# Performance work log

Measured on AMD Instinct MI355X. Metric: run time of the kernel, lower is better.

Reference implementation:

```python
import jax, jax.numpy as jnp
import numpy as np

B, S, F = 128, 256, 40
H, D, NH, L, FF = 64, 128, 4, 2, 2048
REG, BIN, NW = 8, 1, 3
NEG = -1e9


def _ln(x, s, b, eps=1e-5):
    m = x.mean(-1, keepdims=True)
    v = ((x - m) ** 2).mean(-1, keepdims=True)
    return (x - m) / jnp.sqrt(v + eps) * s + b


def setup_inputs() -> dict:
    key = jax.random.key(0)
    ks = list(jax.random.split(key, 40))
    k = iter(ks)
    def rn(shape, s=0.05):
        return jax.random.normal(next(k), shape, jnp.float32) * s
    inp = {}
    inp['x'] = jax.random.normal(next(k), (B, S, F), jnp.float32)
    inp['mask'] = jnp.ones((B, S, F), jnp.float32)
    inp['delta'] = jax.random.uniform(next(k), (B, S, F), jnp.float32)
    # GRU params (torch layout: [3H, in], gates order r,z,n)
    inp['gru_w_ih'] = rn((3 * H, 3 * F))
    inp['gru_w_hh'] = rn((3 * H, H))
    inp['gru_b_ih'] = rn((3 * H,))
    inp['gru_b_hh'] = rn((3 * H,))
    inp['dm_w'] = rn((D, H)); inp['dm_b'] = rn((D,))
    # transformer layers stacked on leading dim L
    inp['in_proj_w'] = rn((L, 3 * D, D)); inp['in_proj_b'] = rn((L, 3 * D))
    inp['out_proj_w'] = rn((L, D, D)); inp['out_proj_b'] = rn((L, D))
    inp['lin1_w'] = rn((L, FF, D)); inp['lin1_b'] = rn((L, FF))
    inp['lin2_w'] = rn((L, D, FF)); inp['lin2_b'] = rn((L, D))
    inp['ln1_s'] = jnp.ones((L, D), jnp.float32); inp['ln1_b'] = jnp.zeros((L, D), jnp.float32)
    inp['ln2_s'] = jnp.ones((L, D), jnp.float32); inp['ln2_b'] = jnp.zeros((L, D), jnp.float32)
    inp['score_w'] = rn((1, D)); inp['score_b'] = rn((1,))
    inp['reg_w'] = rn((NW, REG, D)); inp['reg_b'] = rn((NW, REG))
    inp['bin_w'] = rn((NW, BIN, D)); inp['bin_b'] = rn((NW, BIN))
    inp['window_id'] = jax.random.randint(next(k), (B,), 0, NW, jnp.int32)
    return inp


def reference(x, mask, delta, gru_w_ih, gru_w_hh, gru_b_ih, gru_b_hh, dm_w, dm_b,
              in_proj_w, in_proj_b, out_proj_w, out_proj_b, lin1_w, lin1_b,
              lin2_w, lin2_b, ln1_s, ln1_b, ln2_s, ln2_b, score_w, score_b,
              reg_w, reg_b, bin_w, bin_b, window_id):
    inp = jnp.concatenate([x, mask, delta], -1)          # [B,S,3F]
    xw = inp @ gru_w_ih.T + gru_b_ih                      # [B,S,3H] precomputed input gates

    def step(h, xw_t):
        gh = h @ gru_w_hh.T + gru_b_hh
        xr, xz, xn = jnp.split(xw_t, 3, -1)
        hr, hz, hn = jnp.split(gh, 3, -1)
        r = jax.nn.sigmoid(xr + hr)
        zg = jax.nn.sigmoid(xz + hz)
        n = jnp.tanh(xn + r * hn)
        h_new = (1.0 - zg) * n + zg * h
        return h_new, h_new

    h0 = jnp.zeros((x.shape[0], H), x.dtype)
    _, hs = jax.lax.scan(step, h0, jnp.swapaxes(xw, 0, 1))  # [S,B,H]
    z = jnp.swapaxes(hs, 0, 1) @ dm_w.T + dm_b              # [B,S,D]

    time_mask = mask.sum(-1) > 0                            # [B,S] bool
    bias = jnp.where(time_mask[:, None, None, :], 0.0, NEG).astype(z.dtype)
    dh = D // NH
    scale = 1.0 / np.sqrt(dh)

    for l in range(L):  # post-LN torch TransformerEncoderLayer
        qkv = z @ in_proj_w[l].T + in_proj_b[l]
        q, k, v = jnp.split(qkv, 3, -1)
        q = q.reshape(B, S, NH, dh).transpose(0, 2, 1, 3)
        k = k.reshape(B, S, NH, dh).transpose(0, 2, 1, 3)
        v = v.reshape(B, S, NH, dh).transpose(0, 2, 1, 3)
        attn = jax.nn.softmax(jnp.einsum('bhqd,bhkd->bhqk', q, k) * scale + bias, -1)
        o = jnp.einsum('bhqk,bhkd->bhqd', attn, v).transpose(0, 2, 1, 3).reshape(B, S, D)
        z = _ln(z + (o @ out_proj_w[l].T + out_proj_b[l]), ln1_s[l], ln1_b[l])
        ff = jax.nn.relu(z @ lin1_w[l].T + lin1_b[l]) @ lin2_w[l].T + lin2_b[l]
        z = _ln(z + ff, ln2_s[l], ln2_b[l])

    scores = (z @ score_w.T + score_b)[..., 0]              # [B,S]
    scores = jnp.where(time_mask, scores, NEG)
    alpha = jax.nn.softmax(scores, 1)
    pooled = jnp.einsum('bsd,bs->bd', z, alpha)             # [B,D]

    # routed heads: gather 1-of-3 head weights per sample, batched matvec
    y_reg = jnp.einsum('bod,bd->bo', reg_w[window_id], pooled) + reg_b[window_id]
    y_bin = jnp.einsum('bod,bd->bo', bin_w[window_id], pooled) + bin_b[window_id]
    return (y_reg, y_bin)
```

## Files before the change

kernel.cpp:

```cpp
#include <hip/hip_runtime.h>

typedef __attribute__((ext_vector_type(8))) short short8;
typedef __attribute__((ext_vector_type(4))) float f32x4;
typedef unsigned short u16;

#define BB   128
#define SS   256
#define FIN  40
#define HH   64
#define DD   128
#define NHH  4
#define LL   2
#define NEGV (-1e9f)

__device__ __forceinline__ u16 f2b(float f) {
    unsigned u = __float_as_uint(f);
    return (u16)((u + 0x7FFFu + ((u >> 16) & 1u)) >> 16);
}
__device__ __forceinline__ float b2f(u16 u) {
    return __uint_as_float(((unsigned)u) << 16);
}

__device__ __forceinline__ void gl_lds16(const void* g, void* s) {
    __builtin_amdgcn_global_load_lds(
        (const __attribute__((address_space(1))) void*)g,
        (__attribute__((address_space(3))) void*)s, 16, 0, 0);
}

__global__ __launch_bounds__(192) void xw_kernel(const float* __restrict__ x,
                                                 const float* __restrict__ mask,
                                                 const float* __restrict__ delta,
                                                 const float* __restrict__ w_ih,
                                                 const float* __restrict__ b_ih,
                                                 float* __restrict__ xwt) {
    __shared__ float inp[16][120];
    __shared__ float wl[192][21];
    int group = blockIdx.x >> 8;
    int t = blockIdx.x & 255;
    int tid = threadIdx.x;

    for (int idx = tid; idx < 16 * 120; idx += 192) {
        int r = idx / 120, k = idx % 120;
        size_t g = (size_t)(group * 16 + r) * 256 + t;
        float v;
        if (k < 40)      v = x[g * FIN + k];
        else if (k < 80) v = mask[g * FIN + (k - 40)];
        else             v = delta[g * FIN + (k - 80)];
        inp[r][k] = v;
    }

    float acc[16];
#pragma unroll
    for (int r = 0; r < 16; ++r) acc[r] = 0.f;

    for (int kt = 0; kt < 6; ++kt) {
        __syncthreads();
        for (int idx = tid; idx < 192 * 20; idx += 192) {
            int r = idx / 20, k = idx % 20;
            wl[r][k] = w_ih[(size_t)r * 120 + kt * 20 + k];
        }
        __syncthreads();
#pragma unroll
        for (int kk = 0; kk < 20; ++kk) {
            float w = wl[tid][kk];
            int kg = kt * 20 + kk;
#pragma unroll
            for (int r = 0; r < 16; ++r) acc[r] += w * inp[r][kg];
        }
    }
    float bias = b_ih[tid];
    float* o = xwt + ((size_t)(group * 256 + t) * 192 + tid) * 16;
#pragma unroll
    for (int r = 0; r < 16; r += 4) {
        float4 v = {acc[r] + bias, acc[r + 1] + bias, acc[r + 2] + bias, acc[r + 3] + bias};
        *(float4*)&o[r] = v;
    }
}

__device__ __forceinline__ float gru_gate(float xr, float xz, float xn,
                                          float ar, float az, float an, float hold) {
    float r  = 1.f / (1.f + __expf(-(xr + ar)));
    float zg = 1.f / (1.f + __expf(-(xz + az)));
    float nx = xn + r * an;
    float n  = 2.f / (1.f + __expf(-2.f * nx)) - 1.f;
    return (1.f - zg) * n + zg * hold;
}

__global__ __launch_bounds__(512, 1) void pre_kernel(const float* __restrict__ w_hh,
                                                     const float* __restrict__ b_hh,
                                                     const float* __restrict__ xwt,
                                                     u16* __restrict__ hsb,
                                                     const float* __restrict__ dm_w,
                                                     const float* __restrict__ ip_w,
                                                     const float* __restrict__ op_w,
                                                     const float* __restrict__ l1_w,
                                                     const float* __restrict__ l2_w,
                                                     u16* __restrict__ o_dm, u16* __restrict__ o_ip,
                                                     u16* __restrict__ o_op, u16* __restrict__ o_l1,
                                                     u16* __restrict__ o_l2,
                                                     const float* __restrict__ mask,
                                                     float* __restrict__ tm) {
    __shared__ __align__(16) u16 hb[2][16 * 64];
    __shared__ __align__(16) u16 hstage[8][16 * 64];
    int blk = blockIdx.x;
    int tid = threadIdx.x;

    if (blk >= 8) {
        if (blk < 298) {
            int cb = blk - 8;
            const float* s; u16* d; int off;
            if      (cb < 2)   { s = dm_w; d = o_dm; off = cb; }
            else if (cb < 26)  { s = ip_w; d = o_ip; off = cb - 2; }
            else if (cb < 34)  { s = op_w; d = o_op; off = cb - 26; }
            else if (cb < 162) { s = l1_w; d = o_l1; off = cb - 34; }
            else               { s = l2_w; d = o_l2; off = cb - 162; }
            int i = (off * 512 + tid) * 8;
            float4 a = *(const float4*)&s[i];
            float4 b = *(const float4*)&s[i + 4];
            short8 o;
            o[0] = (short)f2b(a.x); o[1] = (short)f2b(a.y); o[2] = (short)f2b(a.z); o[3] = (short)f2b(a.w);
            o[4] = (short)f2b(b.x); o[5] = (short)f2b(b.y); o[6] = (short)f2b(b.z); o[7] = (short)f2b(b.w);
            *(short8*)&d[i] = o;
        } else {
            int row = (blk - 298) * 512 + tid;
            if (row < BB * SS) {
                const float* m = mask + (size_t)row * FIN;
                float s = 0.f;
                for (int f = 0; f < FIN; ++f) s += m[f];
                tm[row] = (s > 0.f) ? 1.f : 0.f;
            }
        }
        return;
    }

    int b0 = blk * 16;
    int w = tid >> 6, lane = tid & 63;
    int fr = lane & 15, hi = lane >> 4;
    int cw = w & 3;
    int jg = w >> 2;

    for (int idx = tid; idx < 1024; idx += 512) hb[0][idx] = 0;

    int c = cw * 16 + fr;
    float br_ = b_hh[c], bz_ = b_hh[64 + c], bn_ = b_hh[128 + c];

    short8 wfr[2], wfz[2], wfn[2];
#pragma unroll
    for (int ks = 0; ks < 2; ++ks) {
        int slot = ks * 4 + hi;
        const float* p0 = w_hh + (size_t)c * 64 + slot * 8;
        const float* p1 = w_hh + (size_t)(64 + c) * 64 + slot * 8;
        const float* p2 = w_hh + (size_t)(128 + c) * 64 + slot * 8;
#pragma unroll
        for (int q = 0; q < 8; ++q) {
            wfr[ks][q] = (short)f2b(p0[q]);
            wfz[ks][q] = (short)f2b(p1[q]);
            wfn[ks][q] = (short)f2b(p2[q]);
        }
    }

    const float* xg = xwt + (size_t)blk * (256 * 192 * 16);
    int lo = hi * 4 + jg * 2;

    float hrA = 0.f, hrB = 0.f;

    int woA = (lo + 0) * 64 + ((((c >> 3) ^ ((lo + 0) & 7))) << 3) + (c & 7);
    int woB = (lo + 1) * 64 + ((((c >> 3) ^ ((lo + 1) & 7))) << 3) + (c & 7);
    int soA = (lo + 0) * 64 + c;
    int soB = (lo + 1) * 64 + c;

    float2 pxr[4], pxz[4], pxn[4];
#pragma unroll
    for (int u = 0; u < 4; ++u) {
        pxr[u] = *(const float2*)&xg[((size_t)u * 192 + c) * 16 + lo];
        pxz[u] = *(const float2*)&xg[((size_t)u * 192 + 64 + c) * 16 + lo];
        pxn[u] = *(const float2*)&xg[((size_t)u * 192 + 128 + c) * 16 + lo];
    }
    __syncthreads();

    int cur = 0;
    auto step = [&](float2 xr2, float2 xz2, float2 xn2, int ts) {
        f32x4 ar = {br_, br_, br_, br_};
        f32x4 az = {bz_, bz_, bz_, bz_};
        f32x4 an = {bn_, bn_, bn_, bn_};
#pragma unroll
        for (int ks = 0; ks < 2; ++ks) {
            int soff = (((ks << 2) + hi) ^ (fr & 7)) << 3;
            short8 af = *(const short8*)&hb[cur][fr * 64 + soff];
            ar = __builtin_amdgcn_mfma_f32_16x16x32_bf16(af, wfr[ks], ar, 0, 0, 0);
            az = __builtin_amdgcn_mfma_f32_16x16x32_bf16(af, wfz[ks], az, 0, 0, 0);
            an = __builtin_amdgcn_mfma_f32_16x16x32_bf16(af, wfn[ks], an, 0, 0, 0);
        }
        float aR0, aR1, aZ0, aZ1, aN0, aN1;
        if (jg == 0) { aR0 = ar[0]; aR1 = ar[1]; aZ0 = az[0]; aZ1 = az[1]; aN0 = an[0]; aN1 = an[1]; }
        else         { aR0 = ar[2]; aR1 = ar[3]; aZ0 = az[2]; aZ1 = az[3]; aN0 = an[2]; aN1 = an[3]; }
        hrA = gru_gate(xr2.x, xz2.x, xn2.x, aR0, aZ0, aN0, hrA);
        hrB = gru_gate(xr2.y, xz2.y, xn2.y, aR1, aZ1, aN1, hrB);
        u16 v0 = f2b(hrA), v1 = f2b(hrB);
        int nxt = cur ^ 1;
        hb[nxt][woA] = v0; hb[nxt][woB] = v1;
        hstage[ts][soA] = v0; hstage[ts][soB] = v1;
        asm volatile("s_waitcnt lgkmcnt(0)\n\ts_barrier" ::: "memory");
        cur = nxt;
    };

    for (int t = 0; t < SS; t += 8) {
#pragma unroll
        for (int u = 0; u < 8; ++u) {
            int tp = t + u + 4; tp = (tp < SS) ? tp : (SS - 1);
            float2 nr = *(const float2*)&xg[((size_t)tp * 192 + c) * 16 + lo];
            float2 nz = *(const float2*)&xg[((size_t)tp * 192 + 64 + c) * 16 + lo];
            float2 nn = *(const float2*)&xg[((size_t)tp * 192 + 128 + c) * 16 + lo];
            step(pxr[u & 3], pxz[u & 3], pxn[u & 3], u);
            pxr[u & 3] = nr; pxz[u & 3] = nz; pxn[u & 3] = nn;
        }
#pragma unroll
        for (int f = 0; f < 2; ++f) {
            int idx = tid + f * 512;
            int c8 = idx & 7, pair = idx >> 3;
            int ts = pair >> 4, row = pair & 15;
            short8 v = *(const short8*)&hstage[ts][row * 64 + c8 * 8];
            *(short8*)&hsb[((size_t)(b0 + row) * SS + t + ts) * 64 + c8 * 8] = v;
        }
        asm volatile("s_waitcnt lgkmcnt(0)\n\ts_barrier" ::: "memory");
    }
}

template <int MODE, bool RELU>
__global__ __launch_bounds__(256, 2) void mfma_gemm(const u16* __restrict__ A,
                                                    const u16* __restrict__ W,
                                                    const float* __restrict__ bias,
                                                    float* __restrict__ C,
                                                    u16* __restrict__ Cb,
                                                    int M, int N, int K) {
    __shared__ __align__(16) u16 Al[128 * 64];
    __shared__ __align__(16) u16 Bl[128 * 64];
    int bm = blockIdx.x, bn = blockIdx.y;
    int tid = threadIdx.x;
    int w = tid >> 6, lane = tid & 63;
    int wrow = (w >> 1) * 64, wcol = (w & 1) * 64;
    int fr = lane & 15, hi = lane >> 4;
    int rl = lane >> 3;
    int sl = lane & 7;
    int ssl = sl ^ rl;

    const u16* Ag = A + ((size_t)bm * 128) * K + ssl * 8;
    const u16* Wg = W + ((size_t)bn * 128) * K + ssl * 8;

    f32x4 acc[4][4];
#pragma unroll
    for (int i = 0; i < 4; ++i)
#pragma unroll
        for (int jj = 0; jj < 4; ++jj) acc[i][jj] = (f32x4){0.f, 0.f, 0.f, 0.f};

    int ar[4], br[4];
#pragma unroll
    for (int m = 0; m < 4; ++m) {
        ar[m] = (wrow + m * 16 + fr) * 64;
        br[m] = (wcol + m * 16 + fr) * 64;
    }
    int swz = (fr & 7);

    for (int kt = 0; kt < K; kt += 64) {
        __syncthreads();
#pragma unroll
        for (int i = 0; i < 4; ++i) {
            int c = w * 4 + i;
            int row = c * 8 + rl;
            gl_lds16(Ag + (size_t)row * K + kt, &Al[c * 512]);
            gl_lds16(Wg + (size_t)row * K + kt, &Bl[c * 512]);
        }
        __syncthreads();
#pragma unroll
        for (int kk = 0; kk < 2; ++kk) {
            short8 a[4], bq[4];
            int soff = (((kk << 2) + hi) ^ swz) << 3;
#pragma unroll
            for (int m = 0; m < 4; ++m)
                a[m] = *(const short8*)&Al[ar[m] + soff];
#pragma unroll
            for (int n = 0; n < 4; ++n)
                bq[n] = *(const short8*)&Bl[br[n] + soff];
#pragma unroll
            for (int m = 0; m < 4; ++m)
#pragma unroll
                for (int n = 0; n < 4; ++n)
                    acc[m][n] = __builtin_amdgcn_mfma_f32_16x16x32_bf16(a[m], bq[n], acc[m][n], 0, 0, 0);
        }
    }

    float bv[4];
#pragma unroll
    for (int n = 0; n < 4; ++n) bv[n] = bias[bn * 128 + wcol + n * 16 + fr];

#pragma unroll
    for (int m = 0; m < 4; ++m) {
#pragma unroll
        for (int j = 0; j < 4; ++j) {
            int row = bm * 128 + wrow + m * 16 + hi * 4 + j;
#pragma unroll
            for (int n = 0; n < 4; ++n) {
                int col = bn * 128 + wcol + n * 16 + fr;
                float vv = acc[m][n][j] + bv[n];
                if (RELU) vv = fmaxf(vv, 0.f);
                if (MODE & 1) C[(size_t)row * N + col] = vv;
                if (MODE & 2) Cb[(size_t)row * N + col] = f2b(vv);
            }
        }
    }
}

__global__ __launch_bounds__(256, 1) void tail_kernel(const u16* __restrict__ attnob,
                                                      const u16* __restrict__ opw,
                                                      const float* __restrict__ opb,
                                                      const float* __restrict__ ln1s,
                                                      const float* __restrict__ ln1b,
                                                      const u16* __restrict__ w1,
                                                      const float* __restrict__ b1,
                                                      const u16* __restrict__ w2,
                                                      const float* __restrict__ b2,
                                                      const float* __restrict__ lns,
                                                      const float* __restrict__ lnb,
                                                      float* __restrict__ z,
                                                      u16* __restrict__ zbout) {
    __shared__ __align__(16) u16 ZB[2][128 * 64];
    __shared__ __align__(16) u16 W1C[2][128 * 64];
    __shared__ __align__(16) u16 W2C[2][128 * 64];
    __shared__ __align__(16) u16 A1[2][128 * 64];
    __shared__ float lred[2][2][128];
    int bm = blockIdx.x;
    int tid = threadIdx.x;
    int w = tid >> 6, lane = tid & 63;
    int wrow = (w >> 1) * 64, wcol = (w & 1) * 64;
    int fr = lane & 15, hi = lane >> 4;
    int rl = lane >> 3, ssl = (lane & 7) ^ rl;
    int swz = fr & 7;
    int xh = wrow >> 6;

#pragma unroll
    for (int hk = 0; hk < 2; ++hk)
#pragma unroll
        for (int i = 0; i < 4; ++i) {
            int ch = w * 4 + i, row = ch * 8 + rl;
            gl_lds16(attnob + ((size_t)(bm * 128 + row)) * 128 + hk * 64 + ssl * 8, &ZB[hk][ch * 512]);
            gl_lds16(opw + ((size_t)row) * 128 + hk * 64 + ssl * 8, &W1C[hk][ch * 512]);
        }
    __syncthreads();

    {
        f32x4 acc1[4][4];
#pragma unroll
        for (int m = 0; m < 4; ++m)
#pragma unroll
            for (int n = 0; n < 4; ++n) acc1[m][n] = (f32x4){0.f, 0.f, 0.f, 0.f};
#pragma unroll
        for (int ks = 0; ks < 4; ++ks) {
            int hk = ks >> 1;
            int soff = ((((ks & 1) << 2) + hi) ^ swz) << 3;
            short8 a[4], b[4];
#pragma unroll
            for (int m = 0; m < 4; ++m)
                a[m] = *(const short8*)&ZB[hk][(wrow + m * 16 + fr) * 64 + soff];
#pragma unroll
            for (int n = 0; n < 4; ++n)
                b[n] = *(const short8*)&W1C[hk][(wcol + n * 16 + fr) * 64 + soff];
#pragma unroll
            for (int m = 0; m < 4; ++m)
#pragma unroll
                for (int n = 0; n < 4; ++n)
                    acc1[m][n] = __builtin_amdgcn_mfma_f32_16x16x32_bf16(a[m], b[n], acc1[m][n], 0, 0, 0);
        }

        float bv[4];
#pragma unroll
        for (int n = 0; n < 4; ++n) bv[n] = opb[wcol + n * 16 + fr];
        float v[4][4][4];
#pragma unroll
        for (int m = 0; m < 4; ++m)
#pragma unroll
            for (int j = 0; j < 4; ++j) {
                int row = bm * 128 + wrow + m * 16 + hi * 4 + j;
#pragma unroll
                for (int n = 0; n < 4; ++n)
                    v[m][n][j] = acc1[m][n][j] + bv[n] + z[(size_t)row * 128 + wcol + n * 16 + fr];
            }
#pragma unroll
        for (int m = 0; m < 4; ++m)
#pragma unroll
            for (int j = 0; j < 4; ++j) {
                float s = v[m][0][j] + v[m][1][j] + v[m][2][j] + v[m][3][j];
                float q = v[m][0][j]*v[m][0][j] + v[m][1][j]*v[m][1][j]
                        + v[m][2][j]*v[m][2][j] + v[m][3][j]*v[m][3][j];
#pragma unroll
                for (int off = 1; off <= 8; off <<= 1) {
                    s += __shfl_xor(s, off);
                    q += __shfl_xor(q, off);
                }
                if (fr == 0) {
                    int lrow = wrow + m * 16 + hi * 4 + j;
                    lred[0][w & 1][lrow] = s;
                    lred[1][w & 1][lrow] = q;
                }
            }
        __syncthreads();
        float sv[4], bb[4];
#pragma unroll
        for (int n = 0; n < 4; ++n) {
            sv[n] = ln1s[wcol + n * 16 + fr];
            bb[n] = ln1b[wcol + n * 16 + fr];
        }
#pragma unroll
        for (int m = 0; m < 4; ++m)
#pragma unroll
            for (int j = 0; j < 4; ++j) {
                int lrow = wrow + m * 16 + hi * 4 + j;
                float mean = (lred[0][0][lrow] + lred[0][1][lrow]) * (1.f / 128.f);
                float msq  = (lred[1][0][lrow] + lred[1][1][lrow]) * (1.f / 128.f);
                float rstd = rsqrtf(msq - mean * mean + 1e-5f);
                int row = bm * 128 + lrow;
#pragma unroll
                for (int n = 0; n < 4; ++n) {
                    int col = wcol + n * 16 + fr;
                    float o = (v[m][n][j] - mean) * rstd * sv[n] + bb[n];
                    z[(size_t)row * 128 + col] = o;
                    int e = col & 63;
                    ZB[col >> 6][lrow * 64 + ((((e >> 3) ^ (lrow & 7))) << 3) + (e & 7)] = f2b(o);
                }
            }
    }
    __syncthreads();

    f32x4 acc2[4][4];
#pragma unroll
    for (int m = 0; m < 4; ++m)
#pragma unroll
        for (int n = 0; n < 4; ++n) acc2[m][n] = (f32x4){0.f, 0.f, 0.f, 0.f};

    for (int ci = 0; ci < 16; ++ci) {
#pragma unroll
        for (int hk = 0; hk < 2; ++hk)
#pragma unroll
            for (int i = 0; i < 4; ++i) {
                int ch = w * 4 + i, row = ch * 8 + rl;
                gl_lds16(w1 + ((size_t)(ci * 128 + row)) * 128 + hk * 64 + ssl * 8, &W1C[hk][ch * 512]);
                gl_lds16(w2 + ((size_t)row) * 2048 + ci * 128 + hk * 64 + ssl * 8, &W2C[hk][ch * 512]);
            }
        __syncthreads();

        f32x4 acc1[4][4];
#pragma unroll
        for (int m = 0; m < 4; ++m)
#pragma unroll
            for (int n = 0; n < 4; ++n) acc1[m][n] = (f32x4){0.f, 0.f, 0.f, 0.f};
#pragma unroll
        for (int ks = 0; ks < 4; ++ks) {
            int hk = ks >> 1;
            int soff = ((((ks & 1) << 2) + hi) ^ swz) << 3;
            short8 a[4], b[4];
#pragma unroll
            for (int m = 0; m < 4; ++m)
                a[m] = *(const short8*)&W1C[hk][(wrow + m * 16 + fr) * 64 + soff];
#pragma unroll
            for (int n = 0; n < 4; ++n)
                b[n] = *(const short8*)&ZB[hk][(wcol + n * 16 + fr) * 64 + soff];
#pragma unroll
            for (int m = 0; m < 4; ++m)
#pragma unroll
                for (int n = 0; n < 4; ++n)
                    acc1[m][n] = __builtin_amdgcn_mfma_f32_16x16x32_bf16(a[m], b[n], acc1[m][n], 0, 0, 0);
        }
#pragma unroll
        for (int m = 0; m < 4; ++m) {
            int x0 = wrow + m * 16 + hi * 4;
            float4 bb = *(const float4*)&b1[ci * 128 + x0];
            int slot = (x0 & 63) >> 3;
            int wadd = x0 & 7;
#pragma unroll
            for (int n = 0; n < 4; ++n) {
                int r = wcol + n * 16 + fr;
                float v0 = fmaxf(acc1[m][n][0] + bb.x, 0.f);
                float v1 = fmaxf(acc1[m][n][1] + bb.y, 0.f);
                float v2 = fmaxf(acc1[m][n][2] + bb.z, 0.f);
                float v3 = fmaxf(acc1[m][n][3] + bb.w, 0.f);
                uint2 pk;
                pk.x = (unsigned)f2b(v0) | ((unsigned)f2b(v1) << 16);
                pk.y = (unsigned)f2b(v2) | ((unsigned)f2b(v3) << 16);
                *(uint2*)&A1[xh][r * 64 + ((slot ^ (r & 7)) << 3) + wadd] = pk;
            }
        }
        __syncthreads();

#pragma unroll
        for (int ks = 0; ks < 4; ++ks) {
            int hk = ks >> 1;
            int soff = ((((ks & 1) << 2) + hi) ^ swz) << 3;
            short8 a[4], b[4];
#pragma unroll
            for (int m = 0; m < 4; ++m)
                a[m] = *(const short8*)&W2C[hk][(wrow + m * 16 + fr) * 64 + soff];
#pragma unroll
            for (int n = 0; n < 4; ++n)
                b[n] = *(const short8*)&A1[hk][(wcol + n * 16 + fr) * 64 + soff];
#pragma unroll
            for (int m = 0; m < 4; ++m)
#pragma unroll
                for (int n = 0; n < 4; ++n)
                    acc2[m][n] = __builtin_amdgcn_mfma_f32_16x16x32_bf16(a[m], b[n], acc2[m][n], 0, 0, 0);
        }
        __syncthreads();
    }

    float vv[4][4][4];
#pragma unroll
    for (int m = 0; m < 4; ++m) {
        int x0 = wrow + m * 16 + hi * 4;
        float4 bb = *(const float4*)&b2[x0];
#pragma unroll
        for (int n = 0; n < 4; ++n) {
            int y = wcol + n * 16 + fr;
            float4 zo = *(const float4*)&z[((size_t)(bm * 128 + y)) * 128 + x0];
            vv[m][n][0] = acc2[m][n][0] + bb.x + zo.x;
            vv[m][n][1] = acc2[m][n][1] + bb.y + zo.y;
            vv[m][n][2] = acc2[m][n][2] + bb.z + zo.z;
            vv[m][n][3] = acc2[m][n][3] + bb.w + zo.w;
        }
    }
#pragma unroll
    for (int n = 0; n < 4; ++n) {
        float s = 0.f, q = 0.f;
#pragma unroll
        for (int m = 0; m < 4; ++m)
#pragma unroll
            for (int j = 0; j < 4; ++j) { float v = vv[m][n][j]; s += v; q += v * v; }
        s += __shfl_xor(s, 16); s += __shfl_xor(s, 32);
        q += __shfl_xor(q, 16); q += __shfl_xor(q, 32);
        if (hi == 0) {
            int y = wcol + n * 16 + fr;
            lred[0][xh][y] = s;
            lred[1][xh][y] = q;
        }
    }
    __syncthreads();
#pragma unroll
    for (int n = 0; n < 4; ++n) {
        int y = wcol + n * 16 + fr;
        float mean = (lred[0][0][y] + lred[0][1][y]) * (1.f / 128.f);
        float msq  = (lred[1][0][y] + lred[1][1][y]) * (1.f / 128.f);
        float rstd = rsqrtf(msq - mean * mean + 1e-5f);
#pragma unroll
        for (int m = 0; m < 4; ++m) {
            int x0 = wrow + m * 16 + hi * 4;
            float4 sv = *(const float4*)&lns[x0];
            float4 bv = *(const float4*)&lnb[x0];
            float o0 = (vv[m][n][0] - mean) * rstd * sv.x + bv.x;
            float o1 = (vv[m][n][1] - mean) * rstd * sv.y + bv.y;
            float o2 = (vv[m][n][2] - mean) * rstd * sv.z + bv.z;
            float o3 = (vv[m][n][3] - mean) * rstd * sv.w + bv.w;
            size_t zoff = ((size_t)(bm * 128 + y)) * 128 + x0;
            *(float4*)&z[zoff] = (float4){o0, o1, o2, o3};
            uint2 pk;
            pk.x = (unsigned)f2b(o0) | ((unsigned)f2b(o1) << 16);
            pk.y = (unsigned)f2b(o2) | ((unsigned)f2b(o3) << 16);
            *(uint2*)&zbout[zoff] = pk;
        }
    }
}

__global__ __launch_bounds__(256) void attn_mfma_kernel(const u16* __restrict__ qkv,
                                                        const float* __restrict__ tm,
                                                        u16* __restrict__ attno) {
    __shared__ __align__(16) u16 Kl[256 * 40];
    __shared__ __align__(16) u16 Vt[32 * 264];
    __shared__ __align__(16) u16 Pl[4][64 * 72];
    __shared__ float tmb[256];
    int bh = blockIdx.x;
    int b = bh >> 2, hd = bh & 3;
    int tid = threadIdx.x;
    int w = tid >> 6, lane = tid & 63;
    int fr = lane & 15, hi = lane >> 4;
    const u16* base = qkv + (size_t)b * SS * 384 + hd * 32;

    for (int idx = tid; idx < 1024; idx += 256) {
        int r = idx >> 2, s = idx & 3;
        short8 v = *(const short8*)(base + (size_t)r * 384 + 128 + s * 8);
        *(short8*)&Kl[r * 40 + s * 8] = v;
    }
    for (int idx = tid; idx < 1024; idx += 256) {
        int r = idx >> 2, s = idx & 3;
        short8 v = *(const short8*)(base + (size_t)r * 384 + 256 + s * 8);
#pragma unroll
        for (int q = 0; q < 8; ++q) Vt[(s * 8 + q) * 264 + r] = (u16)v[q];
    }
    tmb[tid] = (tm[b * SS + tid] > 0.f) ? 0.f : NEGV;

    int q0 = w * 64;
    short8 qf[4];
#pragma unroll
    for (int m = 0; m < 4; ++m)
        qf[m] = *(const short8*)(base + (size_t)(q0 + m * 16 + fr) * 384 + hi * 8);
    __syncthreads();

    const float scale = 0.17677669529663687f;
    f32x4 accO[4][2];
#pragma unroll
    for (int m = 0; m < 4; ++m) {
        accO[m][0] = (f32x4){0.f, 0.f, 0.f, 0.f};
        accO[m][1] = (f32x4){0.f, 0.f, 0.f, 0.f};
    }
    float den[4][4];
#pragma unroll
    for (int m = 0; m < 4; ++m)
#pragma unroll
        for (int j = 0; j < 4; ++j) den[m][j] = 0.f;

    u16* pw = &Pl[w][0];

    for (int kt = 0; kt < 4; ++kt) {
        f32x4 accS[4][4];
#pragma unroll
        for (int m = 0; m < 4; ++m)
#pragma unroll
            for (int n = 0; n < 4; ++n) accS[m][n] = (f32x4){0.f, 0.f, 0.f, 0.f};
        short8 kf[4];
#pragma unroll
        for (int n = 0; n < 4; ++n)
            kf[n] = *(const short8*)&Kl[(kt * 64 + n * 16 + fr) * 40 + hi * 8];
#pragma unroll
        for (int m = 0; m < 4; ++m)
#pragma unroll
            for (int n = 0; n < 4; ++n)
                accS[m][n] = __builtin_amdgcn_mfma_f32_16x16x32_bf16(qf[m], kf[n], accS[m][n], 0, 0, 0);

        float bias[4];
#pragma unroll
        for (int n = 0; n < 4; ++n) bias[n] = tmb[kt * 64 + n * 16 + fr];

#pragma unroll
        for (int m = 0; m < 4; ++m) {
            float rs0 = 0.f, rs1 = 0.f, rs2 = 0.f, rs3 = 0.f;
#pragma unroll
            for (int n = 0; n < 4; ++n) {
                float p0 = __expf(accS[m][n][0] * scale + bias[n]);
                float p1 = __expf(accS[m][n][1] * scale + bias[n]);
                float p2 = __expf(accS[m][n][2] * scale + bias[n]);
                float p3 = __expf(accS[m][n][3] * scale + bias[n]);
                rs0 += p0; rs1 += p1; rs2 += p2; rs3 += p3;
                int cb = n * 16 + fr;
                pw[(m * 16 + hi * 4 + 0) * 72 + cb] = f2b(p0);
                pw[(m * 16 + hi * 4 + 1) * 72 + cb] = f2b(p1);
                pw[(m * 16 + hi * 4 + 2) * 72 + cb] = f2b(p2);
                pw[(m * 16 + hi * 4 + 3) * 72 + cb] = f2b(p3);
            }
#pragma unroll
            for (int off = 1; off <= 8; off <<= 1) {
                rs0 += __shfl_xor(rs0, off);
                rs1 += __shfl_xor(rs1, off);
                rs2 += __shfl_xor(rs2, off);
                rs3 += __shfl_xor(rs3, off);
            }
            den[m][0] += rs0; den[m][1] += rs1; den[m][2] += rs2; den[m][3] += rs3;
        }
        asm volatile("s_waitcnt lgkmcnt(0)" ::: "memory");

#pragma unroll
        for (int ks = 0; ks < 2; ++ks) {
            short8 pf[4], vf[2];
#pragma unroll
            for (int m = 0; m < 4; ++m)
                pf[m] = *(const short8*)&pw[(m * 16 + fr) * 72 + ks * 32 + hi * 8];
#pragma unroll
            for (int nd = 0; nd < 2; ++nd)
                vf[nd] = *(const short8*)&Vt[(nd * 16 + fr) * 264 + kt * 64 + ks * 32 + hi * 8];
#pragma unroll
            for (int m = 0; m < 4; ++m)
#pragma unroll
                for (int nd = 0; nd < 2; ++nd)
                    accO[m][nd] = __builtin_amdgcn_mfma_f32_16x16x32_bf16(pf[m], vf[nd], accO[m][nd], 0, 0, 0);
        }
    }

    u16* orow = attno + (size_t)(b * SS + q0) * DD + hd * 32;
#pragma unroll
    for (int m = 0; m < 4; ++m)
#pragma unroll
        for (int j = 0; j < 4; ++j) {
            float inv = 1.f / den[m][j];
            int qr = m * 16 + hi * 4 + j;
            orow[(size_t)qr * DD + fr]      = f2b(accO[m][0][j] * inv);
            orow[(size_t)qr * DD + 16 + fr] = f2b(accO[m][1][j] * inv);
        }
}

__global__ __launch_bounds__(256) void pool_all_kernel(const float* __restrict__ z,
                                                       const float* __restrict__ score_w,
                                                       const float* __restrict__ score_b,
                                                       const float* __restrict__ tm,
                                                       const float* __restrict__ reg_w,
                                                       const float* __restrict__ reg_b,
                                                       const float* __restrict__ bin_w,
                                                       const float* __restrict__ bin_b,
                                                       const int* __restrict__ wid,
                                                       float* __restrict__ out) {
    int b = blockIdx.x;
    int tid = threadIdx.x;
    __shared__ float sw[128];
    __shared__ float al[SS];
    __shared__ float red[8];
    __shared__ float pp[2][128];
    __shared__ float p[128];

    if (tid < 128) sw[tid] = score_w[tid];
    __syncthreads();

    const float* zr = z + ((size_t)b * SS + tid) * DD;
    float acc = 0.f;
#pragma unroll
    for (int j = 0; j < 128; j += 4) {
        float4 a = *(const float4*)&zr[j];
        float4 wv = *(const float4*)&sw[j];
        acc += a.x * wv.x + a.y * wv.y + a.z * wv.z + a.w * wv.w;
    }
    float sc = acc + score_b[0];
    sc = (tm[b * SS + tid] > 0.f) ? sc : NEGV;

    float m = sc;
#pragma unroll
    for (int off = 32; off; off >>= 1) m = fmaxf(m, __shfl_xor(m, off));
    if ((tid & 63) == 0) red[tid >> 6] = m;
    __syncthreads();
    m = fmaxf(fmaxf(red[0], red[1]), fmaxf(red[2], red[3]));
    float e = __expf(sc - m);
    float ssum = e;
#pragma unroll
    for (int off = 32; off; off >>= 1) ssum += __shfl_xor(ssum, off);
    if ((tid & 63) == 0) red[4 + (tid >> 6)] = ssum;
    __syncthreads();
    ssum = red[4] + red[5] + red[6] + red[7];
    al[tid] = e / ssum;
    __syncthreads();

    int d = tid & 127, half = tid >> 7;
    float pa = 0.f;
    for (int t = half; t < SS; t += 2) pa += al[t] * z[((size_t)b * SS + t) * DD + d];
    pp[half][d] = pa;
    __syncthreads();
    if (tid < 128) p[tid] = pp[0][tid] + pp[1][tid];
    __syncthreads();

    if (tid < 9) {
        int wi = wid[b];
        const float* wrow;
        float bias;
        if (tid < 8) { wrow = reg_w + ((size_t)wi * 8 + tid) * 128; bias = reg_b[wi * 8 + tid]; }
        else         { wrow = bin_w + (size_t)wi * 128;             bias = bin_b[wi]; }
        float hacc = bias;
        for (int k = 0; k < 128; ++k) hacc += wrow[k] * p[k];
        if (tid < 8) out[b * 8 + tid] = hacc;
        else         out[1024 + b] = hacc;
    }
}

extern "C" void kernel_launch(void* const* d_in, const int* in_sizes, int n_in,
                              void* d_out, int out_size, void* d_ws, size_t ws_size,
                              hipStream_t stream) {
    const float* x         = (const float*)d_in[0];
    const float* mask      = (const float*)d_in[1];
    const float* delta     = (const float*)d_in[2];
    const float* gru_w_ih  = (const float*)d_in[3];
    const float* gru_w_hh  = (const float*)d_in[4];
    const float* gru_b_ih  = (const float*)d_in[5];
    const float* gru_b_hh  = (const float*)d_in[6];
    const float* dm_w      = (const float*)d_in[7];
    const float* dm_b      = (const float*)d_in[8];
    const float* in_proj_w = (const float*)d_in[9];
    const float* in_proj_b = (const float*)d_in[10];
    const float* out_proj_w= (const float*)d_in[11];
    const float* out_proj_b= (const float*)d_in[12];
    const float* lin1_w    = (const float*)d_in[13];
    const float* lin1_b    = (const float*)d_in[14];
    const float* lin2_w    = (const float*)d_in[15];
    const float* lin2_b    = (const float*)d_in[16];
    const float* ln1_s     = (const float*)d_in[17];
    const float* ln1_bb    = (const float*)d_in[18];
    const float* ln2_s     = (const float*)d_in[19];
    const float* ln2_bb    = (const float*)d_in[20];
    const float* score_w   = (const float*)d_in[21];
    const float* score_b   = (const float*)d_in[22];
    const float* reg_w     = (const float*)d_in[23];
    const float* reg_b     = (const float*)d_in[24];
    const float* bin_w     = (const float*)d_in[25];
    const float* bin_b     = (const float*)d_in[26];
    const int*   window_id = (const int*)d_in[27];
    float* out = (float*)d_out;

    char* w8 = (char*)d_ws;
    float* z      = (float*)(w8 + 0);
    u16*   zb     = (u16*)  (w8 + 16777216);
    u16*   hsb    = (u16*)  (w8 + 25165824);
    u16*   wb_dm  = (u16*)  (w8 + 29360128);
    u16*   wb_ip  = (u16*)  (w8 + 29376512);
    u16*   wb_op  = (u16*)  (w8 + 29573120);
    u16*   wb_l1  = (u16*)  (w8 + 29638656);
    u16*   wb_l2  = (u16*)  (w8 + 30687232);
    float* tm     = (float*)(w8 + 31735808);
    float* xwt    = (float*)(w8 + 32063488);
    u16*   qkvb   = (u16*)  (w8 + 32063488);
    u16*   attnob = (u16*)  (w8 + 57229312);

    xw_kernel<<<2048, 192, 0, stream>>>(x, mask, delta, gru_w_ih, gru_b_ih, xwt);
    pre_kernel<<<362, 512, 0, stream>>>(gru_w_hh, gru_b_hh, xwt, hsb,
                                        dm_w, in_proj_w, out_proj_w, lin1_w, lin2_w,
                                        wb_dm, wb_ip, wb_op, wb_l1, wb_l2, mask, tm);

    mfma_gemm<3, false><<<dim3(256, 1), 256, 0, stream>>>(
        hsb, wb_dm, dm_b, z, zb, 32768, 128, 64);

    for (int l = 0; l < LL; ++l) {
        mfma_gemm<2, false><<<dim3(256, 3), 256, 0, stream>>>(
            zb, wb_ip + (size_t)l * 49152, in_proj_b + l * 384, nullptr, qkvb, 32768, 384, 128);
        attn_mfma_kernel<<<BB * NHH, 256, 0, stream>>>(qkvb, tm, attnob);
        tail_kernel<<<256, 256, 0, stream>>>(
            attnob, wb_op + (size_t)l * 16384, out_proj_b + l * 128,
            ln1_s + l * 128, ln1_bb + l * 128,
            wb_l1 + (size_t)l * 262144, lin1_b + l * 2048,
            wb_l2 + (size_t)l * 262144, lin2_b + l * 128,
            ln2_s + l * 128, ln2_bb + l * 128, z, zb);
    }

    pool_all_kernel<<<BB, 256, 0, stream>>>(z, score_w, score_b, tm,
                                            reg_w, reg_b, bin_w, bin_b, window_id, out);
}
```

Before: 487.4 us.

## Fuse QKV projection into preceding dm-projection and tail kernels

The separate QKV GEMM launches are folded into the kernels that produce z. The dm projection kernel now computes the layer-0 QKV directly from its LDS-resident bf16 output. The layer-0 tail kernel computes the layer-1 QKV after the layer norm, writing the swizzled bf16 z tile into LDS instead of to a global bf16 buffer. This removes the global zb round trip and two kernel launches, at the cost of running the three QKV column blocks serially inside one 256-block grid at occupancy 1, which lowers parallelism for that GEMM.

```diff
diff --git a/kernel.cpp b/kernel.cpp
--- a/kernel.cpp
+++ b/kernel.cpp
@@ -226,103 +226,138 @@
     }
 }
 
-template <int MODE, bool RELU>
-__global__ __launch_bounds__(256, 2) void mfma_gemm(const u16* __restrict__ A,
-                                                    const u16* __restrict__ W,
-                                                    const float* __restrict__ bias,
-                                                    float* __restrict__ C,
-                                                    u16* __restrict__ Cb,
-                                                    int M, int N, int K) {
-    __shared__ __align__(16) u16 Al[128 * 64];
-    __shared__ __align__(16) u16 Bl[128 * 64];
-    int bm = blockIdx.x, bn = blockIdx.y;
+__global__ __launch_bounds__(256, 1) void dmqkv_kernel(const u16* __restrict__ hsb,
+                                                       const u16* __restrict__ dmw,
+                                                       const float* __restrict__ dmb,
+                                                       const u16* __restrict__ ipw,
+                                                       const float* __restrict__ ipb,
+                                                       float* __restrict__ z,
+                                                       u16* __restrict__ qkvb) {
+    __shared__ __align__(16) u16 ZB[2][128 * 64];
+    __shared__ __align__(16) u16 W1C[2][128 * 64];
+    int bm = blockIdx.x;
     int tid = threadIdx.x;
     int w = tid >> 6, lane = tid & 63;
     int wrow = (w >> 1) * 64, wcol = (w & 1) * 64;
     int fr = lane & 15, hi = lane >> 4;
-    int rl = lane >> 3;
-    int sl = lane & 7;
-    int ssl = sl ^ rl;
-
-    const u16* Ag = A + ((size_t)bm * 128) * K + ssl * 8;
-    const u16* Wg = W + ((size_t)bn * 128) * K + ssl * 8;
+    int rl = lane >> 3, ssl = (lane & 7) ^ rl;
+    int swz = fr & 7;
+
+#pragma unroll
+    for (int i = 0; i < 4; ++i) {
+        int ch = w * 4 + i, row = ch * 8 + rl;
+        gl_lds16(hsb + ((size_t)(bm * 128 + row)) * 64 + ssl * 8, &ZB[0][ch * 512]);
+        gl_lds16(dmw + ((size_t)row) * 64 + ssl * 8, &W1C[0][ch * 512]);
+    }
+    __syncthreads();
 
     f32x4 acc[4][4];
 #pragma unroll
-    for (int i = 0; i < 4; ++i)
-#pragma unroll
-        for (int jj = 0; jj < 4; ++jj) acc[i][jj] = (f32x4){0.f, 0.f, 0.f, 0.f};
-
-    int ar[4], br[4];
-#pragma unroll
-    for (int m = 0; m < 4; ++m) {
-        ar[m] = (wrow + m * 16 + fr) * 64;
-        br[m] = (wcol + m * 16 + fr) * 64;
-    }
-    int swz = (fr & 7);
-
-    for (int kt = 0; kt < K; kt += 64) {
+    for (int m = 0; m < 4; ++m)
+#pragma unroll
+        for (int n = 0; n < 4; ++n) acc[m][n] = (f32x4){0.f, 0.f, 0.f, 0.f};
+#pragma unroll
+    for (int kk = 0; kk < 2; ++kk) {
+        int soff = (((kk << 2) + hi) ^ swz) << 3;
+        short8 a[4], b[4];
+#pragma unroll
+        for (int m = 0; m < 4; ++m)
+            a[m] = *(const short8*)&ZB[0][(wrow + m * 16 + fr) * 64 + soff];
+#pragma unroll
+        for (int n = 0; n < 4; ++n)
+            b[n] = *(const short8*)&W1C[0][(wcol + n * 16 + fr) * 64 + soff];
+#pragma unroll
+        for (int m = 0; m < 4; ++m)
+#pragma unroll
+            for (int n = 0; n < 4; ++n)
+                acc[m][n] = __builtin_amdgcn_mfma_f32_16x16x32_bf16(a[m], b[n], acc[m][n], 0, 0, 0);
+    }
+    __syncthreads();
+
+    float bv[4];
+#pragma unroll
+    for (int n = 0; n < 4; ++n) bv[n] = dmb[wcol + n * 16 + fr];
+#pragma unroll
+    for (int m = 0; m < 4; ++m)
+#pragma unroll
+        for (int j = 0; j < 4; ++j) {
+            int lrow = wrow + m * 16 + hi * 4 + j;
+            int row = bm * 128 + lrow;
+#pragma unroll
+            for (int n = 0; n < 4; ++n) {
+                int col = wcol + n * 16 + fr;
+                float o = acc[m][n][j] + bv[n];
+                z[(size_t)row * 128 + col] = o;
+                int e = col & 63;
+                ZB[col >> 6][lrow * 64 + ((((e >> 3) ^ (lrow & 7))) << 3) + (e & 7)] = f2b(o);
+            }
+        }
+    __syncthreads();
+
+    for (int bn = 0; bn < 3; ++bn) {
+#pragma unroll
+        for (int hk = 0; hk < 2; ++hk)
+#pragma unroll
+            for (int i = 0; i < 4; ++i) {
+                int ch = w * 4 + i, row = ch * 8 + rl;
+                gl_lds16(ipw + ((size_t)(bn * 128 + row)) * 128 + hk * 64 + ssl * 8, &W1C[hk][ch * 512]);
+            }
         __syncthreads();
-#pragma unroll
-        for (int i = 0; i < 4; ++i) {
-            int c = w * 4 + i;
-            int row = c * 8 + rl;
-            gl_lds16(Ag + (size_t)row * K + kt, &Al[c * 512]);
-            gl_lds16(Wg + (size_t)row * K + kt, &Bl[c * 512]);
-        }
+
+        f32x4 aq[4][4];
+#pragma unroll
+        for (int m = 0; m < 4; ++m)
+#pragma unroll
+            for (int n = 0; n < 4; ++n) aq[m][n] = (f32x4){0.f, 0.f, 0.f, 0.f};
+#pragma unroll
+        for (int ks = 0; ks < 4; ++ks) {
+            int hk = ks >> 1;
+            int soff = ((((ks & 1) << 2) + hi) ^ swz) << 3;
+            short8 a[4], b[4];
+#pragma unroll
+            for (int m = 0; m < 4; ++m)
+                a[m] = *(const short8*)&ZB[hk][(wrow + m * 16 + fr) * 64 + soff];
+#pragma unroll
+            for (int n = 0; n < 4; ++n)
+                b[n] = *(const short8*)&W1C[hk][(wcol + n * 16 + fr) * 64 + soff];
+#pragma unroll
+            for (int m = 0; m < 4; ++m)
+#pragma unroll
+                for (int n = 0; n < 4; ++n)
+                    aq[m][n] = __builtin_amdgcn_mfma_f32_16x16x32_bf16(a[m], b[n], aq[m][n], 0, 0, 0);
+        }
+        float qb[4];
+#pragma unroll
+        for (int n = 0; n < 4; ++n) qb[n] = ipb[bn * 128 + wcol + n * 16 + fr];
+#pragma unroll
+        for (int m = 0; m < 4; ++m)
+#pragma unroll
+            for (int j = 0; j < 4; ++j) {
+                int row = bm * 128 + wrow + m * 16 + hi * 4 + j;
+#pragma unroll
+                for (int n = 0; n < 4; ++n)
+                    qkvb[(size_t)row * 384 + bn * 128 + wcol + n * 16 + fr] = f2b(aq[m][n][j] + qb[n]);
+            }
         __syncthreads();
-#pragma unroll
-        for (int kk = 0; kk < 2; ++kk) {
-            short8 a[4], bq[4];
-            int soff = (((kk << 2) + hi) ^ swz) << 3;
-#pragma unroll
-            for (int m = 0; m < 4; ++m)
-                a[m] = *(const short8*)&Al[ar[m] + soff];
-#pragma unroll
-            for (int n = 0; n < 4; ++n)
-                bq[n] = *(const short8*)&Bl[br[n] + soff];
-#pragma unroll
-            for (int m = 0; m < 4; ++m)
-#pragma unroll
-                for (int n = 0; n < 4; ++n)
-                    acc[m][n] = __builtin_amdgcn_mfma_f32_16x16x32_bf16(a[m], bq[n], acc[m][n], 0, 0, 0);
-        }
-    }
-
-    float bv[4];
-#pragma unroll
-    for (int n = 0; n < 4; ++n) bv[n] = bias[bn * 128 + wcol + n * 16 + fr];
-
-#pragma unroll
-    for (int m = 0; m < 4; ++m) {
-#pragma unroll
-        for (int j = 0; j < 4; ++j) {
-            int row = bm * 128 + wrow + m * 16 + hi * 4 + j;
-#pragma unroll
-            for (int n = 0; n < 4; ++n) {
-                int col = bn * 128 + wcol + n * 16 + fr;
-                float vv = acc[m][n][j] + bv[n];
-                if (RELU) vv = fmaxf(vv, 0.f);
-                if (MODE & 1) C[(size_t)row * N + col] = vv;
-                if (MODE & 2) Cb[(size_t)row * N + col] = f2b(vv);
-            }
-        }
-    }
-}
-
-__global__ __launch_bounds__(256, 1) void tail_kernel(const u16* __restrict__ attnob,
-                                                      const u16* __restrict__ opw,
-                                                      const float* __restrict__ opb,
-                                                      const float* __restrict__ ln1s,
-                                                      const float* __restrict__ ln1b,
-                                                      const u16* __restrict__ w1,
-                                                      const float* __restrict__ b1,
-                                                      const u16* __restrict__ w2,
-                                                      const float* __restrict__ b2,
-                                                      const float* __restrict__ lns,
-                                                      const float* __restrict__ lnb,
-                                                      float* __restrict__ z,
-                                                      u16* __restrict__ zbout) {
+    }
+}
+
+template <bool DO_QKV>
+__global__ __launch_bounds__(256, 1) void tailqkv_kernel(const u16* __restrict__ attnob,
+                                                         const u16* __restrict__ opw,
+                                                         const float* __restrict__ opb,
+                                                         const float* __restrict__ ln1s,
+                                                         const float* __restrict__ ln1b,
+                                                         const u16* __restrict__ w1,
+                                                         const float* __restrict__ b1,
+                                                         const u16* __restrict__ w2,
+                                                         const float* __restrict__ b2,
+                                                         const float* __restrict__ lns,
+                                                         const float* __restrict__ lnb,
+                                                         const u16* __restrict__ ipw,
+                                                         const float* __restrict__ ipb,
+                                                         float* __restrict__ z,
+                                                         u16* __restrict__ qkvb) {
     __shared__ __align__(16) u16 ZB[2][128 * 64];
     __shared__ __align__(16) u16 W1C[2][128 * 64];
     __shared__ __align__(16) u16 W2C[2][128 * 64];
@@ -558,10 +593,65 @@
             float o3 = (vv[m][n][3] - mean) * rstd * sv.w + bv.w;
             size_t zoff = ((size_t)(bm * 128 + y)) * 128 + x0;
             *(float4*)&z[zoff] = (float4){o0, o1, o2, o3};
-            uint2 pk;
-            pk.x = (unsigned)f2b(o0) | ((unsigned)f2b(o1) << 16);
-            pk.y = (unsigned)f2b(o2) | ((unsigned)f2b(o3) << 16);
-            *(uint2*)&zbout[zoff] = pk;
+            if (DO_QKV) {
+#pragma unroll
+                for (int j = 0; j < 4; ++j) {
+                    int col = x0 + j;
+                    int e = col & 63;
+                    float ov = (j == 0) ? o0 : (j == 1) ? o1 : (j == 2) ? o2 : o3;
+                    ZB[col >> 6][y * 64 + ((((e >> 3) ^ (y & 7))) << 3) + (e & 7)] = f2b(ov);
+                }
+            }
+        }
+    }
+
+    if (DO_QKV) {
+        __syncthreads();
+        for (int bn = 0; bn < 3; ++bn) {
+#pragma unroll
+            for (int hk = 0; hk < 2; ++hk)
+#pragma unroll
+                for (int i = 0; i < 4; ++i) {
+                    int ch = w * 4 + i, row = ch * 8 + rl;
+                    gl_lds16(ipw + ((size_t)(bn * 128 + row)) * 128 + hk * 64 + ssl * 8, &W1C[hk][ch * 512]);
+                }
+            __syncthreads();
+
+            f32x4 aq[4][4];
+#pragma unroll
+            for (int m = 0; m < 4; ++m)
+#pragma unroll
+                for (int n = 0; n < 4; ++n) aq[m][n] = (f32x4){0.f, 0.f, 0.f, 0.f};
+#pragma unroll
+            for (int ks = 0; ks < 4; ++ks) {
+                int hk = ks >> 1;
+                int soff = ((((ks & 1) << 2) + hi) ^ swz) << 3;
+                short8 a[4], b[4];
+#pragma unroll
+                for (int m = 0; m < 4; ++m)
+                    a[m] = *(const short8*)&ZB[hk][(wrow + m * 16 + fr) * 64 + soff];
+#pragma unroll
+                for (int n = 0; n < 4; ++n)
+                    b[n] = *(const short8*)&W1C[hk][(wcol + n * 16 + fr) * 64 + soff];
+#pragma unroll
+                for (int m = 0; m < 4; ++m)
+#pragma unroll
+                    for (int n = 0; n < 4; ++n)
+                        aq[m][n] = __builtin_amdgcn_mfma_f32_16x16x32_bf16(a[m], b[n], aq[m][n], 0, 0, 0);
+            }
+            float qb[4];
+#pragma unroll
+            for (int n = 0; n < 4; ++n) qb[n] = ipb[bn * 128 + wcol + n * 16 + fr];
+#pragma unroll
+            for (int m = 0; m < 4; ++m)
+#pragma unroll
+                for (int j = 0; j < 4; ++j) {
+                    int row = bm * 128 + wrow + m * 16 + hi * 4 + j;
+#pragma unroll
+                    for (int n = 0; n < 4; ++n)
+                        qkvb[(size_t)row * 384 + bn * 128 + wcol + n * 16 + fr] = f2b(aq[m][n][j] + qb[n]);
+                }
+            __syncthreads();
         }
     }
 }
@@ -795,7 +885,6 @@
 
     char* w8 = (char*)d_ws;
     float* z      = (float*)(w8 + 0);
-    u16*   zb     = (u16*)  (w8 + 16777216);
     u16*   hsb    = (u16*)  (w8 + 25165824);
     u16*   wb_dm  = (u16*)  (w8 + 29360128);
     u16*   wb_ip  = (u16*)  (w8 + 29376512);
@@ -812,20 +901,19 @@
                                         dm_w, in_proj_w, out_proj_w, lin1_w, lin2_w,
                                         wb_dm, wb_ip, wb_op, wb_l1, wb_l2, mask, tm);
 
-    mfma_gemm<3, false><<<dim3(256, 1), 256, 0, stream>>>(
-        hsb, wb_dm, dm_b, z, zb, 32768, 128, 64);
-
-    for (int l = 0; l < LL; ++l) {
-        mfma_gemm<2, false><<<dim3(256, 3), 256, 0, stream>>>(
-            zb, wb_ip + (size_t)l * 49152, in_proj_b + l * 384, nullptr, qkvb, 32768, 384, 128);
-        attn_mfma_kernel<<<BB * NHH, 256, 0, stream>>>(qkvb, tm, attnob);
-        tail_kernel<<<256, 256, 0, stream>>>(
-            attnob, wb_op + (size_t)l * 16384, out_proj_b + l * 128,
-            ln1_s + l * 128, ln1_bb + l * 128,
-            wb_l1 + (size_t)l * 262144, lin1_b + l * 2048,
-            wb_l2 + (size_t)l * 262144, lin2_b + l * 128,
-            ln2_s + l * 128, ln2_bb + l * 128, z, zb);
-    }
+    dmqkv_kernel<<<256, 256, 0, stream>>>(hsb, wb_dm, dm_b, wb_ip, in_proj_b, z, qkvb);
+
+    attn_mfma_kernel<<<BB * NHH, 256, 0, stream>>>(qkvb, tm, attnob);
+    tailqkv_kernel<true><<<256, 256, 0, stream>>>(
+        attnob, wb_op, out_proj_b, ln1_s, ln1_bb,
+        wb_l1, lin1_b, wb_l2, lin2_b, ln2_s, ln2_bb,
+        wb_ip + 49152, in_proj_b + 384, z, qkvb);
+
+    attn_mfma_kernel<<<BB * NHH, 256, 0, stream>>>(qkvb, tm, attnob);
+    tailqkv_kernel<false><<<256, 256, 0, stream>>>(
+        attnob, wb_op + 16384, out_proj_b + 128, ln1_s + 128, ln1_bb + 128,
+        wb_l1 + 262144, lin1_b + 2048, wb_l2 + 262144, lin2_b + 128,
+        ln2_s + 128, ln2_bb + 128, nullptr, nullptr, z, nullptr);
 
     pool_all_kernel<<<BB, 256, 0, stream>>>(z, score_w, score_b, tm,
                                             reg_w, reg_b, bin_w, bin_b, window_id, out);
```

Result: no change. 484.2 us, median of 2 (-0.7%).
